# Kernel optimization log

Measured on AMD Instinct MI355X. Metric: run time of the kernel, lower is better.

The kernel has to match this reference:

```python
import jax, jax.numpy as jnp
import numpy as np

B, D, VOCAB = 8192, 256, 1000000


def setup_inputs() -> dict:
    key = jax.random.key(0)
    k1, k2, k3, k4 = jax.random.split(key, 4)
    input_emb = jax.random.normal(k1, (B, D), dtype=jnp.float32)
    target_emb = jax.random.normal(k2, (B, D), dtype=jnp.float32)
    target_ids = jax.random.randint(k3, (B, 1), 0, VOCAB, dtype=jnp.int64)
    # sampling probabilities must lie strictly in (0,1)
    q_probas = jax.random.uniform(k4, (B,), dtype=jnp.float32) * 0.98 + 0.01
    return {"input_emb": input_emb, "target_emb": target_emb,
            "target_ids": target_ids, "q_probas": q_probas}


def reference(input_emb, target_emb, target_ids, q_probas):
    # sim: [B, B] in-batch similarity
    sim = input_emb @ target_emb.T
    n = q_probas.shape[0]
    # miss[i, j] = True where target j is a valid negative for row i
    miss = target_ids != target_ids.T                      # [B, B] bool
    n_miss = jnp.sum(miss, axis=1, keepdims=True).astype(sim.dtype)  # [B, 1]
    pos_sim = jnp.diagonal(sim)                            # [B]
    # logQ correction: log(n_miss * q_j / (1 - q_i)), broadcast to [B, B]
    correction = jnp.log(n_miss * q_probas[None, :] / (1.0 - q_probas[:, None]))
    mask = miss & (~jnp.eye(n, dtype=bool))                # exclude diagonal
    neg_exp = jnp.where(mask, jnp.exp(sim - correction), 0.0)  # [B, B]
    pos_exp = jnp.exp(pos_sim)
    batch_loss = jnp.mean(-pos_sim + jnp.log(pos_exp + jnp.sum(neg_exp, axis=1)))
    return batch_loss
```

## Files before the change

### kernel.cpp

```cpp
#include <hip/hip_runtime.h>
#include <hip/hip_bf16.h>
#include <stdint.h>

#define MB 8192
#define KD 256
#define BM 128
#define BN 64
#define NSPLIT 8
#define SLAB (MB / NSPLIT)
#define VOCAB 1000000
#define COFF 104.0f

typedef __attribute__((ext_vector_type(8))) short bf16x8;
typedef __attribute__((ext_vector_type(4))) float f32x4;

__device__ __forceinline__ unsigned short f2bf(float x) {
  union { float f; uint32_t u; } v; v.f = x;
  uint32_t r = v.u + 0x7fffu + ((v.u >> 16) & 1u);
  return (unsigned short)(r >> 16);
}

__device__ __forceinline__ float fast_exp(float x) {
#if __has_builtin(__builtin_amdgcn_exp2f)
  return __builtin_amdgcn_exp2f(x * 1.44269504088896340736f);
#else
  return __expf(x);
#endif
}

__global__ __launch_bounds__(256) void convertpos_kernel(
    const float* __restrict__ A, const float* __restrict__ B,
    unsigned short* __restrict__ Abf, unsigned short* __restrict__ Bbf,
    float* __restrict__ pos, int* __restrict__ hist) {
  int t = blockIdx.x * 256 + threadIdx.x;
  const float4 a = ((const float4*)A)[t];
  const float4 b = ((const float4*)B)[t];
  ushort4 oa, ob;
  oa.x = f2bf(a.x); oa.y = f2bf(a.y); oa.z = f2bf(a.z); oa.w = f2bf(a.w);
  ob.x = f2bf(b.x); ob.y = f2bf(b.y); ob.z = f2bf(b.z); ob.w = f2bf(b.w);
  ((ushort4*)Abf)[t] = oa;
  ((ushort4*)Bbf)[t] = ob;
  float d = a.x * b.x + a.y * b.y + a.z * b.z + a.w * b.w;
  #pragma unroll
  for (int off = 32; off; off >>= 1) d += __shfl_down(d, off, 64);
  if ((threadIdx.x & 63) == 0) pos[t >> 6] = d;
  ((uint2*)hist)[t] = make_uint2(0u, 0u);
}

__global__ __launch_bounds__(256) void histb2_kernel(
    const int* __restrict__ ids, const float* __restrict__ q,
    int* __restrict__ hist, float* __restrict__ b2,
    float* __restrict__ ps, float* __restrict__ out) {
  int i = blockIdx.x * 256 + threadIdx.x;
  atomicAdd(&hist[ids[i]], 1);
  b2[i] = -(logf(q[i]) + COFF);
  ps[i] = 0.0f;
  if (i == 0) out[0] = 0.0f;
}

__global__ __launch_bounds__(256, 3) void fused_kernel(
    const unsigned short* __restrict__ Abf,
    const unsigned short* __restrict__ Bbf,
    const int* __restrict__ ids,
    const float* __restrict__ b2,
    float* __restrict__ ps) {
  const int slab = blockIdx.y;
  const int tid = threadIdx.x;
  const int wave = tid >> 6;
  const int lane = tid & 63;
  const int quad = lane >> 4;
  const int lpos = lane & 15;
  const int rowbase = blockIdx.x * BM + wave * 32;

  __shared__ unsigned short Bs[2048 * 8];

  bf16x8 afrag[2][8];
  #pragma unroll
  for (int rt = 0; rt < 2; ++rt)
    #pragma unroll
    for (int kb = 0; kb < 8; ++kb)
      afrag[rt][kb] = *(const bf16x8*)(Abf + (rowbase + rt * 16 + lpos) * KD + kb * 32 + quad * 8);

  int idr[2][4];
  float srun[2][4];
  #pragma unroll
  for (int rt = 0; rt < 2; ++rt)
    #pragma unroll
    for (int r = 0; r < 4; ++r) {
      idr[rt][r] = ids[rowbase + rt * 16 + quad * 4 + r];
      srun[rt][r] = 0.0f;
    }

  for (int ch = 0; ch < SLAB / BN; ++ch) {
    const int colchunk = slab * SLAB + ch * BN;
    __syncthreads();
    #pragma unroll
    for (int s8 = 0; s8 < 8; ++s8) {
      int c = tid + s8 * 256;
      int lp = c & 15, qd = (c >> 4) & 3, kb = (c >> 6) & 7, ct = c >> 9;
      uint4 v = *(const uint4*)(Bbf + (colchunk + ct * 16 + lp) * KD + kb * 32 + qd * 8);
      *(uint4*)(Bs + c * 8) = v;
    }
    __syncthreads();

    #pragma unroll
    for (int ct = 0; ct < 4; ++ct) {
      const unsigned short* bp = Bs + (ct * 512 + quad * 16 + lpos) * 8;
      bf16x8 bfrag[8];
      #pragma unroll
      for (int kb = 0; kb < 8; ++kb)
        bfrag[kb] = *(const bf16x8*)(bp + kb * 512);
      const int j = colchunk + ct * 16 + lpos;
      const int idj = ids[j];
      const float bj = b2[j];
      #pragma unroll
      for (int rt = 0; rt < 2; ++rt) {
        f32x4 acc = {0.0f, 0.0f, 0.0f, 0.0f};
        #pragma unroll
        for (int kb = 0; kb < 8; ++kb)
          acc = __builtin_amdgcn_mfma_f32_16x16x32_bf16(afrag[rt][kb], bfrag[kb], acc, 0, 0, 0);
        #pragma unroll
        for (int r = 0; r < 4; ++r) {
          const float e = fast_exp(acc[r] + bj);
          srun[rt][r] += (idj != idr[rt][r]) ? e : 0.0f;
        }
      }
    }
  }

  #pragma unroll
  for (int rt = 0; rt < 2; ++rt)
    #pragma unroll
    for (int r = 0; r < 4; ++r) {
      float v = srun[rt][r];
      #pragma unroll
      for (int off = 1; off < 16; off <<= 1) v += __shfl_xor(v, off, 64);
      if (lpos == 0)
        atomicAdd(&ps[rowbase + rt * 16 + quad * 4 + r], v);
    }
}

__global__ __launch_bounds__(256) void finalize_kernel(
    const float* __restrict__ ps, const float* __restrict__ pos,
    const float* __restrict__ q, const int* __restrict__ ids,
    const int* __restrict__ hist, float* __restrict__ out) {
  int i = blockIdx.x * 256 + threadIdx.x;
  const float s = ps[i];
  const float nm = (float)(MB - hist[ids[i]]);
  const float z = logf(s) + COFF + logf(1.0f - q[i]) - logf(nm);
  const float p = pos[i];
  const float hi = fmaxf(p, z), lo = fminf(p, z);
  float loss = -p + hi + log1pf(__expf(lo - hi));

  #pragma unroll
  for (int off = 32; off; off >>= 1) loss += __shfl_down(loss, off, 64);
  __shared__ float red[4];
  if ((threadIdx.x & 63) == 0) red[threadIdx.x >> 6] = loss;
  __syncthreads();
  if (threadIdx.x == 0) {
    float t = red[0] + red[1] + red[2] + red[3];
    atomicAdd(out, t * (1.0f / (float)MB));
  }
}

extern "C" void kernel_launch(void* const* d_in, const int* in_sizes, int n_in,
                              void* d_out, int out_size, void* d_ws, size_t ws_size,
                              hipStream_t stream) {
  (void)in_sizes; (void)n_in; (void)out_size; (void)ws_size;
  const float* input_emb  = (const float*)d_in[0];
  const float* target_emb = (const float*)d_in[1];
  const int*   target_ids = (const int*)d_in[2];
  const float* q_probas   = (const float*)d_in[3];
  float* out = (float*)d_out;

  char* ws = (char*)d_ws;
  unsigned short* Abf = (unsigned short*)(ws);
  unsigned short* Bbf = (unsigned short*)(ws + (4u << 20));
  int*   hist = (int*)  (ws + (8u << 20));
  float* b2   = (float*)(ws + (12u << 20));
  float* pos  = (float*)(ws + (12u << 20) + 32768);
  float* ps   = (float*)(ws + (12u << 20) + 65536);

  convertpos_kernel<<<2048, 256, 0, stream>>>(input_emb, target_emb, Abf, Bbf, pos, hist);
  histb2_kernel<<<32, 256, 0, stream>>>(target_ids, q_probas, hist, b2, ps, out);
  fused_kernel<<<dim3(MB / BM, NSPLIT), 256, 0, stream>>>(Abf, Bbf, target_ids, b2, ps);
  finalize_kernel<<<32, 256, 0, stream>>>(ps, pos, q_probas, target_ids, hist, out);
}
```

Baseline: 130.4 us.

## Fuse hist and finalize into GEMM kernel, enlarge row tile, use direct LDS loads

```diff
diff --git a/kernel.cpp b/kernel.cpp
--- a/kernel.cpp
+++ b/kernel.cpp
@@ -1,18 +1,23 @@
 #include <hip/hip_runtime.h>
-#include <hip/hip_bf16.h>
 #include <stdint.h>
 
 #define MB 8192
 #define KD 256
-#define BM 128
+#define BM 256
 #define BN 64
-#define NSPLIT 8
-#define SLAB (MB / NSPLIT)
-#define VOCAB 1000000
+#define NSPLIT 16
+#define SLAB 512
+#define CHUNKS 8
+#define GRIDX 32
+#define NBLOCKS (GRIDX * NSPLIT)
 #define COFF 104.0f
+#define LOG2E 1.44269504088896340736f
 
 typedef __attribute__((ext_vector_type(8))) short bf16x8;
 typedef __attribute__((ext_vector_type(4))) float f32x4;
+
+typedef const __attribute__((address_space(1))) uint32_t* gptr_t;
+typedef __attribute__((address_space(3))) uint32_t* lptr_t;
 
 __device__ __forceinline__ unsigned short f2bf(float x) {
   union { float f; uint32_t u; } v; v.f = x;
@@ -20,18 +25,21 @@
   return (unsigned short)(r >> 16);
 }
 
-__device__ __forceinline__ float fast_exp(float x) {
+__device__ __forceinline__ float fast_exp2(float x) {
 #if __has_builtin(__builtin_amdgcn_exp2f)
-  return __builtin_amdgcn_exp2f(x * 1.44269504088896340736f);
+  return __builtin_amdgcn_exp2f(x);
 #else
-  return __expf(x);
+  return exp2f(x);
 #endif
 }
 
-__global__ __launch_bounds__(256) void convertpos_kernel(
+__global__ __launch_bounds__(256) void prep_kernel(
     const float* __restrict__ A, const float* __restrict__ B,
+    const float* __restrict__ q,
     unsigned short* __restrict__ Abf, unsigned short* __restrict__ Bbf,
-    float* __restrict__ pos, int* __restrict__ hist) {
+    float* __restrict__ b2, float* __restrict__ pos,
+    float* __restrict__ ps, float* __restrict__ pc,
+    unsigned int* __restrict__ counter) {
   int t = blockIdx.x * 256 + threadIdx.x;
   const float4 a = ((const float4*)A)[t];
   const float4 b = ((const float4*)B)[t];
@@ -44,122 +52,142 @@
   #pragma unroll
   for (int off = 32; off; off >>= 1) d += __shfl_down(d, off, 64);
   if ((threadIdx.x & 63) == 0) pos[t >> 6] = d;
-  ((uint2*)hist)[t] = make_uint2(0u, 0u);
-}
-
-__global__ __launch_bounds__(256) void histb2_kernel(
-    const int* __restrict__ ids, const float* __restrict__ q,
-    int* __restrict__ hist, float* __restrict__ b2,
-    float* __restrict__ ps, float* __restrict__ out) {
-  int i = blockIdx.x * 256 + threadIdx.x;
-  atomicAdd(&hist[ids[i]], 1);
-  b2[i] = -(logf(q[i]) + COFF);
-  ps[i] = 0.0f;
-  if (i == 0) out[0] = 0.0f;
-}
-
-__global__ __launch_bounds__(256, 3) void fused_kernel(
+  if (t < MB) {
+    b2[t] = (-logf(q[t]) - COFF) * LOG2E;
+    ps[t] = 0.0f;
+    pc[t] = 0.0f;
+  }
+  if (t == 0) *counter = 0u;
+}
+
+__global__ __launch_bounds__(256, 2) void fused_kernel(
     const unsigned short* __restrict__ Abf,
     const unsigned short* __restrict__ Bbf,
     const int* __restrict__ ids,
     const float* __restrict__ b2,
-    float* __restrict__ ps) {
-  const int slab = blockIdx.y;
+    const float* __restrict__ pos,
+    const float* __restrict__ q,
+    float* __restrict__ ps, float* __restrict__ pc,
+    unsigned int* __restrict__ counter,
+    float* __restrict__ out) {
   const int tid = threadIdx.x;
-  const int wave = tid >> 6;
-  const int lane = tid & 63;
-  const int quad = lane >> 4;
-  const int lpos = lane & 15;
-  const int rowbase = blockIdx.x * BM + wave * 32;
+  const int wave = tid >> 6, lane = tid & 63, quad = lane >> 4, lpos = lane & 15;
+  const int rowbase = blockIdx.x * BM + wave * 64;
+  const int colbase = blockIdx.y * SLAB;
 
   __shared__ unsigned short Bs[2048 * 8];
 
-  bf16x8 afrag[2][8];
-  #pragma unroll
-  for (int rt = 0; rt < 2; ++rt)
+  bf16x8 afrag[4][8];
+  #pragma unroll
+  for (int rt = 0; rt < 4; ++rt)
     #pragma unroll
     for (int kb = 0; kb < 8; ++kb)
-      afrag[rt][kb] = *(const bf16x8*)(Abf + (rowbase + rt * 16 + lpos) * KD + kb * 32 + quad * 8);
-
-  int idr[2][4];
-  float srun[2][4];
-  #pragma unroll
-  for (int rt = 0; rt < 2; ++rt)
+      afrag[rt][kb] = *(const bf16x8*)(Abf + (size_t)(rowbase + rt * 16 + lpos) * KD + kb * 32 + quad * 8);
+
+  int idr[4][4];
+  float srun[4][4];
+  int crun[4];
+  #pragma unroll
+  for (int rt = 0; rt < 4; ++rt) {
+    crun[rt] = 0;
     #pragma unroll
     for (int r = 0; r < 4; ++r) {
       idr[rt][r] = ids[rowbase + rt * 16 + quad * 4 + r];
       srun[rt][r] = 0.0f;
     }
-
-  for (int ch = 0; ch < SLAB / BN; ++ch) {
-    const int colchunk = slab * SLAB + ch * BN;
+  }
+
+  const int lp = tid & 15, qd = (tid >> 4) & 3, kb0 = (tid >> 6) & 3;
+  const unsigned short* srcct[4];
+  #pragma unroll
+  for (int ct = 0; ct < 4; ++ct)
+    srcct[ct] = Bbf + (size_t)(colbase + ct * 16 + lp) * KD + kb0 * 32 + qd * 8;
+
+  for (int ch = 0; ch < CHUNKS; ++ch) {
     __syncthreads();
     #pragma unroll
-    for (int s8 = 0; s8 < 8; ++s8) {
-      int c = tid + s8 * 256;
-      int lp = c & 15, qd = (c >> 4) & 3, kb = (c >> 6) & 7, ct = c >> 9;
-      uint4 v = *(const uint4*)(Bbf + (colchunk + ct * 16 + lp) * KD + kb * 32 + qd * 8);
-      *(uint4*)(Bs + c * 8) = v;
+    for (int ct = 0; ct < 4; ++ct) {
+      #pragma unroll
+      for (int h = 0; h < 2; ++h) {
+        const int s8 = ct * 2 + h;
+        __builtin_amdgcn_global_load_lds(
+            (gptr_t)(const void*)(srcct[ct] + h * 128),
+            (lptr_t)(void*)(Bs + (size_t)(tid + s8 * 256) * 8),
+            16, 0, 0);
+      }
+      srcct[ct] += BN * KD;
     }
     __syncthreads();
 
+    const int colchunk = colbase + ch * BN;
     #pragma unroll
     for (int ct = 0; ct < 4; ++ct) {
-      const unsigned short* bp = Bs + (ct * 512 + quad * 16 + lpos) * 8;
       bf16x8 bfrag[8];
       #pragma unroll
       for (int kb = 0; kb < 8; ++kb)
-        bfrag[kb] = *(const bf16x8*)(bp + kb * 512);
+        bfrag[kb] = *(const bf16x8*)(Bs + (size_t)(ct * 512 + kb * 64 + quad * 16 + lpos) * 8);
+      f32x4 acc[4] = {{0,0,0,0},{0,0,0,0},{0,0,0,0},{0,0,0,0}};
+      #pragma unroll
+      for (int kb = 0; kb < 8; ++kb)
+        #pragma unroll
+        for (int rt = 0; rt < 4; ++rt)
+          acc[rt] = __builtin_amdgcn_mfma_f32_16x16x32_bf16(afrag[rt][kb], bfrag[kb], acc[rt], 0, 0, 0);
       const int j = colchunk + ct * 16 + lpos;
       const int idj = ids[j];
       const float bj = b2[j];
       #pragma unroll
-      for (int rt = 0; rt < 2; ++rt) {
-        f32x4 acc = {0.0f, 0.0f, 0.0f, 0.0f};
-        #pragma unroll
-        for (int kb = 0; kb < 8; ++kb)
-          acc = __builtin_amdgcn_mfma_f32_16x16x32_bf16(afrag[rt][kb], bfrag[kb], acc, 0, 0, 0);
+      for (int rt = 0; rt < 4; ++rt)
         #pragma unroll
         for (int r = 0; r < 4; ++r) {
-          const float e = fast_exp(acc[r] + bj);
-          srun[rt][r] += (idj != idr[rt][r]) ? e : 0.0f;
+          const bool match = (idj == idr[rt][r]);
+          const float x = fmaf(acc[rt][r], LOG2E, bj);
+          srun[rt][r] += fast_exp2(match ? -1000.0f : x);
+          crun[rt] += match ? (1 << (8 * r)) : 0;
         }
+    }
+  }
+
+  #pragma unroll
+  for (int rt = 0; rt < 4; ++rt)
+    #pragma unroll
+    for (int r = 0; r < 4; ++r) {
+      float s = srun[rt][r];
+      float c = (float)((crun[rt] >> (8 * r)) & 255);
+      #pragma unroll
+      for (int off = 1; off < 16; off <<= 1) {
+        s += __shfl_xor(s, off, 64);
+        c += __shfl_xor(c, off, 64);
       }
-    }
-  }
-
-  #pragma unroll
-  for (int rt = 0; rt < 2; ++rt)
-    #pragma unroll
-    for (int r = 0; r < 4; ++r) {
-      float v = srun[rt][r];
-      #pragma unroll
-      for (int off = 1; off < 16; off <<= 1) v += __shfl_xor(v, off, 64);
-      if (lpos == 0)
-        atomicAdd(&ps[rowbase + rt * 16 + quad * 4 + r], v);
-    }
-}
-
-__global__ __launch_bounds__(256) void finalize_kernel(
-    const float* __restrict__ ps, const float* __restrict__ pos,
-    const float* __restrict__ q, const int* __restrict__ ids,
-    const int* __restrict__ hist, float* __restrict__ out) {
-  int i = blockIdx.x * 256 + threadIdx.x;
-  const float s = ps[i];
-  const float nm = (float)(MB - hist[ids[i]]);
-  const float z = logf(s) + COFF + logf(1.0f - q[i]) - logf(nm);
-  const float p = pos[i];
-  const float hi = fmaxf(p, z), lo = fminf(p, z);
-  float loss = -p + hi + log1pf(__expf(lo - hi));
-
-  #pragma unroll
-  for (int off = 32; off; off >>= 1) loss += __shfl_down(loss, off, 64);
-  __shared__ float red[4];
-  if ((threadIdx.x & 63) == 0) red[threadIdx.x >> 6] = loss;
+      if (lpos == 0) {
+        const int gi = rowbase + rt * 16 + quad * 4 + r;
+        atomicAdd(&ps[gi], s);
+        atomicAdd(&pc[gi], c);
+      }
+    }
+
+  __threadfence();
   __syncthreads();
-  if (threadIdx.x == 0) {
-    float t = red[0] + red[1] + red[2] + red[3];
-    atomicAdd(out, t * (1.0f / (float)MB));
+  __shared__ unsigned int done_s;
+  if (tid == 0)
+    done_s = __hip_atomic_fetch_add(counter, 1u, __ATOMIC_ACQ_REL, __HIP_MEMORY_SCOPE_AGENT);
+  __syncthreads();
+  if (done_s == NBLOCKS - 1) {
+    float acc = 0.0f;
+    for (int i = tid; i < MB; i += 256) {
+      const float s  = __hip_atomic_load(&ps[i], __ATOMIC_RELAXED, __HIP_MEMORY_SCOPE_AGENT);
+      const float cm = __hip_atomic_load(&pc[i], __ATOMIC_RELAXED, __HIP_MEMORY_SCOPE_AGENT);
+      const float nm = (float)MB - cm;
+      const float z = logf(s) + COFF + log1pf(-q[i]) - logf(nm);
+      const float p = pos[i];
+      const float hi = fmaxf(p, z), lo = fminf(p, z);
+      acc += -p + hi + log1pf(__expf(lo - hi));
+    }
+    #pragma unroll
+    for (int off = 32; off; off >>= 1) acc += __shfl_down(acc, off, 64);
+    __shared__ float red[4];
+    if (lane == 0) red[wave] = acc;
+    __syncthreads();
+    if (tid == 0) out[0] = (red[0] + red[1] + red[2] + red[3]) * (1.0f / (float)MB);
   }
 }
 
@@ -176,13 +204,14 @@
   char* ws = (char*)d_ws;
   unsigned short* Abf = (unsigned short*)(ws);
   unsigned short* Bbf = (unsigned short*)(ws + (4u << 20));
-  int*   hist = (int*)  (ws + (8u << 20));
-  float* b2   = (float*)(ws + (12u << 20));
-  float* pos  = (float*)(ws + (12u << 20) + 32768);
-  float* ps   = (float*)(ws + (12u << 20) + 65536);
-
-  convertpos_kernel<<<2048, 256, 0, stream>>>(input_emb, target_emb, Abf, Bbf, pos, hist);
-  histb2_kernel<<<32, 256, 0, stream>>>(target_ids, q_probas, hist, b2, ps, out);
-  fused_kernel<<<dim3(MB / BM, NSPLIT), 256, 0, stream>>>(Abf, Bbf, target_ids, b2, ps);
-  finalize_kernel<<<32, 256, 0, stream>>>(ps, pos, q_probas, target_ids, hist, out);
-}
+  float* b2   = (float*)(ws + (8u << 20));
+  float* pos  = (float*)(ws + (8u << 20) + 32768);
+  float* ps   = (float*)(ws + (8u << 20) + 65536);
+  float* pc   = (float*)(ws + (8u << 20) + 98304);
+  unsigned int* counter = (unsigned int*)(ws + (8u << 20) + 131072);
+
+  prep_kernel<<<2048, 256, 0, stream>>>(input_emb, target_emb, q_probas,
+                                        Abf, Bbf, b2, pos, ps, pc, counter);
+  fused_kernel<<<dim3(GRIDX, NSPLIT), 256, 0, stream>>>(
+      Abf, Bbf, target_ids, b2, pos, q_probas, ps, pc, counter, out);
+}
```

Result: slower. 192.4 us (+47.6%).
